# Performance work log

Hardware: AMD Instinct MI355X
Metric: run time of the kernel (lower is better)

Reference implementation:

```python
import jax, jax.numpy as jnp
import numpy as np
from jax import lax

CENTER_NUM = 2048


def setup_inputs() -> dict:
    key = jax.random.key(0)
    xyz = jax.random.normal(key, (32, 65536, 3), dtype=jnp.float32)
    return {"xyz": xyz}


def furthest_point_sample(xyz, m):
    """Iterative FPS. xyz: [B, N, 3] -> indices [B, m] (int32).

    Matches pointnet2_utils.furthest_point_sample: start at index 0,
    maintain running min squared distance to the selected set, pick argmax.
    """
    B, N, _ = xyz.shape
    init_idx = jnp.zeros((B,), dtype=jnp.int32)
    init_dists = jnp.full((B, N), 1e10, dtype=xyz.dtype)

    def step(carry, _):
        dists, last_idx = carry
        last = jnp.take_along_axis(xyz, last_idx[:, None, None], axis=1)  # [B,1,3]
        d = jnp.sum((xyz - last) ** 2, axis=-1)  # [B,N] squared dist to last center
        dists = jnp.minimum(dists, d)
        nxt = jnp.argmax(dists, axis=-1).astype(jnp.int32)  # [B]
        return (dists, nxt), nxt

    (_, _), rest = lax.scan(step, (init_dists, init_idx), None, length=m - 1)
    # rest: [m-1, B] -> prepend initial index, transpose to [B, m]
    idx = jnp.concatenate([init_idx[None, :], rest], axis=0).T
    return idx


def index_points(points, idx):
    """points: [B, N, C], idx: [B, m] -> [B, m, C]."""
    return jnp.take_along_axis(points, idx[..., None], axis=1)


def reference(xyz):
    fps_idx = furthest_point_sample(xyz, CENTER_NUM)  # [B, m]
    center_xyz = index_points(xyz, fps_idx)           # [B, m, 3]
    return center_xyz
```

## Files before the change

kernel.cpp:

```cpp
#include <hip/hip_runtime.h>
#include <stdint.h>

#define NBATCH 32
#define NPTS   65536
#define MCENT  2048
#define BPB    8
#define THREADS 1024
#define CHUNK  (NPTS / BPB)
#define WPT    (CHUNK / THREADS)
#define NWAVE  (THREADS / 64)
#define GPW    2
#define NGRP   (NWAVE * GPW)
#define TMAX   64

typedef unsigned long long u64;
typedef uint32_t u32;

static __device__ __forceinline__ u32 fbits(float f) { union { float f; u32 u; } c; c.f = f; return c.u; }
static __device__ __forceinline__ float bitsf(u32 u) { union { u32 u; float f; } c; c.u = u; return c.f; }

static __device__ __forceinline__ u32 wave_max_u32(u32 v) {
#define STEP(CTRL) { const u32 o = (u32)__builtin_amdgcn_update_dpp(0, (int)v, CTRL, 0xF, 0xF, true); v = o > v ? o : v; }
    STEP(0x111)
    STEP(0x112)
    STEP(0x114)
    STEP(0x118)
    STEP(0x142)
    STEP(0x143)
#undef STEP
    return (u32)__builtin_amdgcn_readlane((int)v, 63);
}


template<int TOPK>
__global__ __launch_bounds__(THREADS, 1) void fps_kernel(
    const float* __restrict__ xyz,
    float* __restrict__ out,
    u64* __restrict__ slots)
{
    constexpr int POOLW = BPB * NGRP * TOPK;
    constexpr int WPL   = POOLW / 64;

    const int t = threadIdx.x;
    const int b = blockIdx.x >> 3;
    const int j = blockIdx.x & 7;
    const float* base = xyz + (size_t)b * NPTS * 3;
    const int p0 = j * CHUNK;
    const int wave = t >> 6;
    const int lane = t & 63;

    float px[WPT], py[WPT], pz[WPT], pd[WPT];
#pragma unroll
    for (int q = 0; q < WPT; ++q) {
        const int p = p0 + q * THREADS + t;
        px[q] = base[(size_t)p * 3 + 0];
        py[q] = base[(size_t)p * 3 + 1];
        pz[q] = base[(size_t)p * 3 + 2];
        pd[q] = 1e10f;
    }

    __shared__ float wcx[TMAX], wcy[TMAX], wcz[TMAX];
    __shared__ int   wcnt;

    if (t == 0) {
        const float cx = base[0], cy = base[1], cz = base[2];
        wcx[0] = cx; wcy[0] = cy; wcz[0] = cz; wcnt = 1;
        if (j == 0) {
            float* o = out + (size_t)b * MCENT * 3;
            o[0] = cx; o[1] = cy; o[2] = cz;
        }
    }

    int C = 0;
    for (int s = 1; ; ++s) {
        __syncthreads();
        const int tn = wcnt;
        C += tn;
        if (C >= MCENT) break;

        for (int tt = 0; tt < tn; ++tt) {
            const float cx = wcx[tt], cy = wcy[tt], cz = wcz[tt];
#pragma unroll
            for (int q = 0; q < WPT; ++q) {
                const float dx = __fsub_rn(px[q], cx);
                const float dy = __fsub_rn(py[q], cy);
                const float dz = __fsub_rn(pz[q], cz);
                const float s2 = __fmaf_rn(dz, dz,
                                 __fmaf_rn(dx, dx,
                                 __fmul_rn(dy, dy)));
                pd[q] = fminf(pd[q], s2);
            }
        }

        u64 k1 = 0, k2 = 0, k3 = 0;
#pragma unroll
        for (int q = 0; q < WPT; ++q) {
            const u64 kk = ((u64)fbits(pd[q]) << 16)
                         | (u64)(0xFFFFu ^ (u32)(p0 + q * THREADS + t));
            if (kk > k1)      { k3 = k2; k2 = k1; k1 = kk; }
            else if (kk > k2) { k3 = k2; k2 = kk; }
            else if (kk > k3) { k3 = kk; }
        }
#pragma unroll
        for (int m = 1; m <= 16; m <<= 1) {
            const u64 o1 = __shfl_xor(k1, m);
            const u64 o2 = __shfl_xor(k2, m);
            if constexpr (TOPK == 2) {
                if (o1 > k1) { k2 = (k1 > o2) ? k1 : o2; k1 = o1; }
                else         { k2 = (k2 > o1) ? k2 : o1; }
            } else {
                const u64 o3 = __shfl_xor(k3, m);
                u64 m1, m2, m3;
                if (o1 > k1) {
                    m1 = o1;
                    if (o2 > k1) { m2 = o2; m3 = (o3 > k1) ? o3 : k1; }
                    else         { m2 = k1; m3 = (o2 > k2) ? o2 : k2; }
                } else {
                    m1 = k1;
                    if (o1 > k2) { m2 = o1; m3 = (o2 > k2) ? o2 : k2; }
                    else         { m2 = k2; m3 = (o1 > k3) ? o1 : k3; }
                }
                k1 = m1; k2 = m2; k3 = m3;
            }
        }

        u64* const bb = slots + ((size_t)(s & 1) * NBATCH + b) * POOLW;
        const u32 tag = (u32)s & 0xFFFFu;

        if ((lane & 31) == 0) {
            const int g = wave * GPW + (lane >> 5);
            u64* const gw = &bb[j * (NGRP * TOPK) + g * TOPK];
            __hip_atomic_store(&gw[0], (k1 << 16) | tag,
                               __ATOMIC_RELAXED, __HIP_MEMORY_SCOPE_AGENT);
            __hip_atomic_store(&gw[1], (k2 << 16) | tag,
                               __ATOMIC_RELAXED, __HIP_MEMORY_SCOPE_AGENT);
            if constexpr (TOPK == 3)
                __hip_atomic_store(&gw[2], (k3 << 16) | tag,
                                   __ATOMIC_RELAXED, __HIP_MEMORY_SCOPE_AGENT);
        }

        if (wave == 0) {
            u64 w[WPL]; int ok;
            do {
#pragma unroll
                for (int r = 0; r < WPL; ++r)
                    w[r] = __hip_atomic_load(&bb[lane + 64 * r],
                                             __ATOMIC_RELAXED, __HIP_MEMORY_SCOPE_AGENT);
                ok = 1;
#pragma unroll
                for (int r = 0; r < WPL; ++r)
                    ok &= ((u32)(w[r] & 0xFFFFull) == tag);
            } while (!__all(ok));

            u32 pv[WPL], pi[WPL];
            float ex[WPL], ey[WPL], ez[WPL];
#pragma unroll
            for (int r = 0; r < WPL; ++r) {
                pv[r] = (u32)(w[r] >> 32);
                pi[r] = ((u32)w[r] >> 16) & 0xFFFFu;
                const int gi = (int)(0xFFFFu ^ pi[r]);
                ex[r] = base[(size_t)gi * 3 + 0];
                ey[r] = base[(size_t)gi * 3 + 1];
                ez[r] = base[(size_t)gi * 3 + 2];
            }

            u32 tl = 0;
#pragma unroll
            for (int r = 0; r < WPL; ++r) {
                const int rank = ((lane % TOPK) + (64 % TOPK) * r) % TOPK;
                if (rank == TOPK - 1) tl = pv[r] > tl ? pv[r] : tl;
            }
            const u32 tauv = wave_max_u32(tl);

            int tc = 0;
            while (1) {
                u32 lv = 0;
#pragma unroll
                for (int r = 0; r < WPL; ++r) lv = pv[r] > lv ? pv[r] : lv;
                const u32 vmax = wave_max_u32(lv);
                if (tc > 0 && vmax <= tauv) break;

                u32 ic = 0;
#pragma unroll
                for (int r = 0; r < WPL; ++r)
                    ic = (pv[r] == vmax && pi[r] + 1u > ic) ? pi[r] + 1u : ic;
                const u64 bal = __ballot(ic != 0);
                u32 winv; int ol;
                if (__popcll(bal) == 1) {
                    ol = (int)__ffsll((long long)bal) - 1;
                    winv = __shfl(ic, ol) - 1u;
                } else {
                    winv = wave_max_u32(ic) - 1u;
                    int m = 0;
#pragma unroll
                    for (int r = 0; r < WPL; ++r)
                        m |= (pv[r] == vmax) & (pi[r] == winv);
                    ol = (int)__ffsll((long long)__ballot(m)) - 1;
                }

                float sx = 0.f, sy = 0.f, sz = 0.f;
#pragma unroll
                for (int r = 0; r < WPL; ++r) {
                    const int m = (pv[r] == vmax) & (pi[r] == winv);
                    sx = m ? ex[r] : sx;
                    sy = m ? ey[r] : sy;
                    sz = m ? ez[r] : sz;
                }
                const float wx = __shfl(sx, ol);
                const float wy = __shfl(sy, ol);
                const float wz = __shfl(sz, ol);

                if (lane == 0) {
                    wcx[tc] = wx; wcy[tc] = wy; wcz[tc] = wz;
                    if (j == 0) {
                        float* o = out + ((size_t)b * MCENT + (C + tc)) * 3;
                        o[0] = wx; o[1] = wy; o[2] = wz;
                    }
                }
                ++tc;
                if (C + tc >= MCENT || tc >= TMAX) break;

#pragma unroll
                for (int r = 0; r < WPL; ++r) {
                    const float dx = __fsub_rn(ex[r], wx);
                    const float dy = __fsub_rn(ey[r], wy);
                    const float dz = __fsub_rn(ez[r], wz);
                    const float s2 = __fmaf_rn(dz, dz,
                                     __fmaf_rn(dx, dx,
                                     __fmul_rn(dy, dy)));
                    pv[r] = fbits(fminf(bitsf(pv[r]), s2));
                }
            }
            if (lane == 0) wcnt = tc;
        }
    }
}

extern "C" void kernel_launch(void* const* d_in, const int* in_sizes, int n_in,
                              void* d_out, int out_size, void* d_ws, size_t ws_size,
                              hipStream_t stream) {
    const float* xyz = (const float*)d_in[0];
    float* out = (float*)d_out;
    u64* slots = (u64*)d_ws;

    const size_t need3 = 2ull * NBATCH * (BPB * NGRP * 3) * sizeof(u64);
    if (ws_size >= need3) {
        fps_kernel<3><<<dim3(NBATCH * BPB), dim3(THREADS), 0, stream>>>(xyz, out, slots);
    } else {
        fps_kernel<2><<<dim3(NBATCH * BPB), dim3(THREADS), 0, stream>>>(xyz, out, slots);
    }
}
```

Before: 2.055 ms.

## Stream centers to waves via tagged shared slots instead of block barrier

Replaces the per-round __syncthreads and the count broadcast with tagged shared-memory slots. Wave 0 publishes each new center as soon as it is selected, and the other waves spin on the slot tags to consume centers incrementally, overlapping their distance updates with wave 0's serial selection. Wave 0 now applies each center to its own points inline. This brings in spin-wait polling on volatile LDS and relies on fence ordering for correctness, so a memory-ordering mistake could cause a hang or wrong results.

Result: slower. 4.959 ms (+141.3%).

```diff
diff --git a/kernel.cpp b/kernel.cpp
--- a/kernel.cpp
+++ b/kernel.cpp
@@ -59,38 +59,66 @@
         pd[q] = 1e10f;
     }
 
-    __shared__ float wcx[TMAX], wcy[TMAX], wcz[TMAX];
-    __shared__ int   wcnt;
-
+    __shared__ volatile float wsx[TMAX], wsy[TMAX], wsz[TMAX];
+    __shared__ volatile u32   wstag[TMAX];
+    __shared__ volatile u32   wtn;
+
+    if (t < TMAX) wstag[t] = 0xFFFFFFFFu;
     if (t == 0) {
-        const float cx = base[0], cy = base[1], cz = base[2];
-        wcx[0] = cx; wcy[0] = cy; wcz[0] = cz; wcnt = 1;
+        wsx[0] = base[0]; wsy[0] = base[1]; wsz[0] = base[2];
+        wstag[0] = 0u;
+        wtn = (0u << 8) | 1u;
         if (j == 0) {
             float* o = out + (size_t)b * MCENT * 3;
-            o[0] = cx; o[1] = cy; o[2] = cz;
-        }
-    }
-
-    int C = 0;
+            o[0] = base[0]; o[1] = base[1]; o[2] = base[2];
+        }
+    }
+    __syncthreads();
+
+    int C;
+    if (wave == 0) {
+        const float cx = base[0], cy = base[1], cz = base[2];
+#pragma unroll
+        for (int q = 0; q < WPT; ++q) {
+            const float dx = __fsub_rn(px[q], cx);
+            const float dy = __fsub_rn(py[q], cy);
+            const float dz = __fsub_rn(pz[q], cz);
+            const float s2 = __fmaf_rn(dz, dz,
+                             __fmaf_rn(dx, dx,
+                             __fmul_rn(dy, dy)));
+            pd[q] = fminf(pd[q], s2);
+        }
+        C = 1;
+    } else {
+        C = 0;
+    }
+
     for (int s = 1; ; ++s) {
-        __syncthreads();
-        const int tn = wcnt;
-        C += tn;
+        if (wave != 0) {
+            int tt = 0, tn = -1;
+            while (tn < 0 || tt < tn) {
+                const u32 tg = wstag[tt];
+                if (tg == (u32)(s - 1)) {
+                    const float cx = wsx[tt], cy = wsy[tt], cz = wsz[tt];
+#pragma unroll
+                    for (int q = 0; q < WPT; ++q) {
+                        const float dx = __fsub_rn(px[q], cx);
+                        const float dy = __fsub_rn(py[q], cy);
+                        const float dz = __fsub_rn(pz[q], cz);
+                        const float s2 = __fmaf_rn(dz, dz,
+                                         __fmaf_rn(dx, dx,
+                                         __fmul_rn(dy, dy)));
+                        pd[q] = fminf(pd[q], s2);
+                    }
+                    ++tt;
+                } else if (tn < 0) {
+                    const u32 wd = wtn;
+                    if ((wd >> 8) == (u32)(s - 1)) tn = (int)(wd & 0xFFu);
+                }
+            }
+            C += tt;
+        }
         if (C >= MCENT) break;
-
-        for (int tt = 0; tt < tn; ++tt) {
-            const float cx = wcx[tt], cy = wcy[tt], cz = wcz[tt];
-#pragma unroll
-            for (int q = 0; q < WPT; ++q) {
-                const float dx = __fsub_rn(px[q], cx);
-                const float dy = __fsub_rn(py[q], cy);
-                const float dz = __fsub_rn(pz[q], cz);
-                const float s2 = __fmaf_rn(dz, dz,
-                                 __fmaf_rn(dx, dx,
-                                 __fmul_rn(dy, dy)));
-                pd[q] = fminf(pd[q], s2);
-            }
-        }
 
         u64 k1 = 0, k2 = 0, k3 = 0;
 #pragma unroll
@@ -211,12 +239,26 @@
                 const float wz = __shfl(sz, ol);
 
                 if (lane == 0) {
-                    wcx[tc] = wx; wcy[tc] = wy; wcz[tc] = wz;
+                    wsx[tc] = wx; wsy[tc] = wy; wsz[tc] = wz;
+                    __threadfence_block();
+                    wstag[tc] = (u32)s;
                     if (j == 0) {
                         float* o = out + ((size_t)b * MCENT + (C + tc)) * 3;
                         o[0] = wx; o[1] = wy; o[2] = wz;
                     }
                 }
+
+#pragma unroll
+                for (int q = 0; q < WPT; ++q) {
+                    const float dx = __fsub_rn(px[q], wx);
+                    const float dy = __fsub_rn(py[q], wy);
+                    const float dz = __fsub_rn(pz[q], wz);
+                    const float s2 = __fmaf_rn(dz, dz,
+                                     __fmaf_rn(dx, dx,
+                                     __fmul_rn(dy, dy)));
+                    pd[q] = fminf(pd[q], s2);
+                }
+
                 ++tc;
                 if (C + tc >= MCENT || tc >= TMAX) break;
 
@@ -231,7 +273,11 @@
                     pv[r] = fbits(fminf(bitsf(pv[r]), s2));
                 }
             }
-            if (lane == 0) wcnt = tc;
+            if (lane == 0) {
+                __threadfence_block();
+                wtn = ((u32)s << 8) | (u32)tc;
+            }
+            C += tc;
         }
     }
 }
```

## Replicate candidate selection across all waves to drop serial wave-0 phase

Applied to the files above, without the earlier changes.

Wave 0 still polls the global candidate slots, but now only copies them into a shared pool. After one barrier, every wave redundantly runs the top-k candidate selection loop. Each wave applies every new center to its own point distances as soon as it is chosen, rather than afterwards from a shared center list. This removes the phase where the other 15 waves sat idle while wave 0 picked centers, and overlaps distance updates with selection. The cost is redundant selection work and more global gathers of candidate coordinates in every wave.

After: 4.080 ms. +98.6%, slower.

```diff
diff --git a/kernel.cpp b/kernel.cpp
--- a/kernel.cpp
+++ b/kernel.cpp
@@ -59,39 +59,29 @@
         pd[q] = 1e10f;
     }
 
-    __shared__ float wcx[TMAX], wcy[TMAX], wcz[TMAX];
-    __shared__ int   wcnt;
-
-    if (t == 0) {
+    __shared__ u64 pool[POOLW];
+
+    if (t == 0 && j == 0) {
+        float* o = out + (size_t)b * MCENT * 3;
+        o[0] = base[0]; o[1] = base[1]; o[2] = base[2];
+    }
+
+    {
         const float cx = base[0], cy = base[1], cz = base[2];
-        wcx[0] = cx; wcy[0] = cy; wcz[0] = cz; wcnt = 1;
-        if (j == 0) {
-            float* o = out + (size_t)b * MCENT * 3;
-            o[0] = cx; o[1] = cy; o[2] = cz;
-        }
-    }
-
-    int C = 0;
+#pragma unroll
+        for (int q = 0; q < WPT; ++q) {
+            const float dx = __fsub_rn(px[q], cx);
+            const float dy = __fsub_rn(py[q], cy);
+            const float dz = __fsub_rn(pz[q], cz);
+            const float s2 = __fmaf_rn(dz, dz,
+                             __fmaf_rn(dx, dx,
+                             __fmul_rn(dy, dy)));
+            pd[q] = fminf(pd[q], s2);
+        }
+    }
+
+    int C = 1;
     for (int s = 1; ; ++s) {
-        __syncthreads();
-        const int tn = wcnt;
-        C += tn;
-        if (C >= MCENT) break;
-
-        for (int tt = 0; tt < tn; ++tt) {
-            const float cx = wcx[tt], cy = wcy[tt], cz = wcz[tt];
-#pragma unroll
-            for (int q = 0; q < WPT; ++q) {
-                const float dx = __fsub_rn(px[q], cx);
-                const float dy = __fsub_rn(py[q], cy);
-                const float dz = __fsub_rn(pz[q], cz);
-                const float s2 = __fmaf_rn(dz, dz,
-                                 __fmaf_rn(dx, dx,
-                                 __fmul_rn(dy, dy)));
-                pd[q] = fminf(pd[q], s2);
-            }
-        }
-
         u64 k1 = 0, k2 = 0, k3 = 0;
 #pragma unroll
         for (int q = 0; q < WPT; ++q) {
@@ -151,88 +141,104 @@
                 for (int r = 0; r < WPL; ++r)
                     ok &= ((u32)(w[r] & 0xFFFFull) == tag);
             } while (!__all(ok));
-
-            u32 pv[WPL], pi[WPL];
-            float ex[WPL], ey[WPL], ez[WPL];
+#pragma unroll
+            for (int r = 0; r < WPL; ++r)
+                pool[lane + 64 * r] = w[r];
+        }
+        __syncthreads();
+
+        u32 pv[WPL], pi[WPL];
+        float ex[WPL], ey[WPL], ez[WPL];
+#pragma unroll
+        for (int r = 0; r < WPL; ++r) {
+            const u64 w = pool[lane + 64 * r];
+            pv[r] = (u32)(w >> 32);
+            pi[r] = ((u32)w >> 16) & 0xFFFFu;
+            const int gi = (int)(0xFFFFu ^ pi[r]);
+            ex[r] = base[(size_t)gi * 3 + 0];
+            ey[r] = base[(size_t)gi * 3 + 1];
+            ez[r] = base[(size_t)gi * 3 + 2];
+        }
+
+        u32 tl = 0;
+#pragma unroll
+        for (int r = 0; r < WPL; ++r) {
+            const int rank = ((lane % TOPK) + (64 % TOPK) * r) % TOPK;
+            if (rank == TOPK - 1) tl = pv[r] > tl ? pv[r] : tl;
+        }
+        const u32 tauv = wave_max_u32(tl);
+
+        int tc = 0;
+        while (1) {
+            u32 lv = 0;
+#pragma unroll
+            for (int r = 0; r < WPL; ++r) lv = pv[r] > lv ? pv[r] : lv;
+            const u32 vmax = wave_max_u32(lv);
+            if (tc > 0 && vmax <= tauv) break;
+
+            u32 ic = 0;
+#pragma unroll
+            for (int r = 0; r < WPL; ++r)
+                ic = (pv[r] == vmax && pi[r] + 1u > ic) ? pi[r] + 1u : ic;
+            const u64 bal = __ballot(ic != 0);
+            u32 winv; int ol;
+            if (__popcll(bal) == 1) {
+                ol = (int)__ffsll((long long)bal) - 1;
+                winv = __shfl(ic, ol) - 1u;
+            } else {
+                winv = wave_max_u32(ic) - 1u;
+                int m = 0;
+#pragma unroll
+                for (int r = 0; r < WPL; ++r)
+                    m |= (pv[r] == vmax) & (pi[r] == winv);
+                ol = (int)__ffsll((long long)__ballot(m)) - 1;
+            }
+
+            float sx = 0.f, sy = 0.f, sz = 0.f;
 #pragma unroll
             for (int r = 0; r < WPL; ++r) {
-                pv[r] = (u32)(w[r] >> 32);
-                pi[r] = ((u32)w[r] >> 16) & 0xFFFFu;
-                const int gi = (int)(0xFFFFu ^ pi[r]);
-                ex[r] = base[(size_t)gi * 3 + 0];
-                ey[r] = base[(size_t)gi * 3 + 1];
-                ez[r] = base[(size_t)gi * 3 + 2];
-            }
-
-            u32 tl = 0;
+                const int m = (pv[r] == vmax) & (pi[r] == winv);
+                sx = m ? ex[r] : sx;
+                sy = m ? ey[r] : sy;
+                sz = m ? ez[r] : sz;
+            }
+            const float wx = __shfl(sx, ol);
+            const float wy = __shfl(sy, ol);
+            const float wz = __shfl(sz, ol);
+
+            if (wave == 0 && lane == 0 && j == 0) {
+                float* o = out + ((size_t)b * MCENT + (C + tc)) * 3;
+                o[0] = wx; o[1] = wy; o[2] = wz;
+            }
+
+#pragma unroll
+            for (int q = 0; q < WPT; ++q) {
+                const float dx = __fsub_rn(px[q], wx);
+                const float dy = __fsub_rn(py[q], wy);
+                const float dz = __fsub_rn(pz[q], wz);
+                const float s2 = __fmaf_rn(dz, dz,
+                                 __fmaf_rn(dx, dx,
+                                 __fmul_rn(dy, dy)));
+                pd[q] = fminf(pd[q], s2);
+            }
+
+            ++tc;
+            if (C + tc >= MCENT || tc >= TMAX) break;
+
 #pragma unroll
             for (int r = 0; r < WPL; ++r) {
-                const int rank = ((lane % TOPK) + (64 % TOPK) * r) % TOPK;
-                if (rank == TOPK - 1) tl = pv[r] > tl ? pv[r] : tl;
-            }
-            const u32 tauv = wave_max_u32(tl);
-
-            int tc = 0;
-            while (1) {
-                u32 lv = 0;
-#pragma unroll
-                for (int r = 0; r < WPL; ++r) lv = pv[r] > lv ? pv[r] : lv;
-                const u32 vmax = wave_max_u32(lv);
-                if (tc > 0 && vmax <= tauv) break;
-
-                u32 ic = 0;
-#pragma unroll
-                for (int r = 0; r < WPL; ++r)
-                    ic = (pv[r] == vmax && pi[r] + 1u > ic) ? pi[r] + 1u : ic;
-                const u64 bal = __ballot(ic != 0);
-                u32 winv; int ol;
-                if (__popcll(bal) == 1) {
-                    ol = (int)__ffsll((long long)bal) - 1;
-                    winv = __shfl(ic, ol) - 1u;
-                } else {
-                    winv = wave_max_u32(ic) - 1u;
-                    int m = 0;
-#pragma unroll
-                    for (int r = 0; r < WPL; ++r)
-                        m |= (pv[r] == vmax) & (pi[r] == winv);
-                    ol = (int)__ffsll((long long)__ballot(m)) - 1;
-                }
-
-                float sx = 0.f, sy = 0.f, sz = 0.f;
-#pragma unroll
-                for (int r = 0; r < WPL; ++r) {
-                    const int m = (pv[r] == vmax) & (pi[r] == winv);
-                    sx = m ? ex[r] : sx;
-                    sy = m ? ey[r] : sy;
-                    sz = m ? ez[r] : sz;
-                }
-                const float wx = __shfl(sx, ol);
-                const float wy = __shfl(sy, ol);
-                const float wz = __shfl(sz, ol);
-
-                if (lane == 0) {
-                    wcx[tc] = wx; wcy[tc] = wy; wcz[tc] = wz;
-                    if (j == 0) {
-                        float* o = out + ((size_t)b * MCENT + (C + tc)) * 3;
-                        o[0] = wx; o[1] = wy; o[2] = wz;
-                    }
-                }
-                ++tc;
-                if (C + tc >= MCENT || tc >= TMAX) break;
-
-#pragma unroll
-                for (int r = 0; r < WPL; ++r) {
-                    const float dx = __fsub_rn(ex[r], wx);
-                    const float dy = __fsub_rn(ey[r], wy);
-                    const float dz = __fsub_rn(ez[r], wz);
-                    const float s2 = __fmaf_rn(dz, dz,
-                                     __fmaf_rn(dx, dx,
-                                     __fmul_rn(dy, dy)));
-                    pv[r] = fbits(fminf(bitsf(pv[r]), s2));
-                }
-            }
-            if (lane == 0) wcnt = tc;
-        }
+                const float dx = __fsub_rn(ex[r], wx);
+                const float dy = __fsub_rn(ey[r], wy);
+                const float dz = __fsub_rn(ez[r], wz);
+                const float s2 = __fmaf_rn(dz, dz,
+                                 __fmaf_rn(dx, dx,
+                                 __fmul_rn(dy, dy)));
+                pv[r] = fbits(fminf(bitsf(pv[r]), s2));
+            }
+        }
+
+        C += tc;
+        if (C >= MCENT) break;
     }
 }
 
```
